# Kernel optimization log

Hardware: AMD Instinct MI355X
Metric: run time of the kernel (lower is better)

Reference implementation:

```python
import jax, jax.numpy as jnp
import numpy as np

H = 56; W = 56; WS = 7; SHIFT = 3; HEADS = 4; DIM = 128
N = WS * WS  # 49 tokens per window
EPS = 1e-5


def _rel_pos_index():
    c = np.stack(np.meshgrid(np.arange(WS), np.arange(WS), indexing='ij')).reshape(2, -1)
    r = (c[:, :, None] - c[:, None, :]).transpose(1, 2, 0)
    r[..., 0] += WS - 1
    r[..., 1] += WS - 1
    r[..., 0] *= 2 * WS - 1
    return jnp.asarray(r.sum(-1))  # [N, N] int


def _attn_mask():
    img = np.zeros((H, W))
    sl = (slice(0, -WS), slice(-WS, -SHIFT), slice(-SHIFT, None))
    cnt = 0
    for hs in sl:
        for ws_ in sl:
            img[hs, ws_] = cnt
            cnt += 1
    mw = img.reshape(H // WS, WS, W // WS, WS).transpose(0, 2, 1, 3).reshape(-1, N)
    d = mw[:, None, :] - mw[:, :, None]  # [nW, N, N]
    return jnp.asarray(np.where(d != 0, -100.0, 0.0).astype(np.float32))


def _ln(x, w, b):
    m = x.mean(-1, keepdims=True)
    v = ((x - m) ** 2).mean(-1, keepdims=True)
    return (x - m) / jnp.sqrt(v + EPS) * w + b


def setup_inputs() -> dict:
    key = jax.random.key(0)
    ks = jax.random.split(key, 8)
    B = 64
    return {
        'x': jax.random.normal(ks[0], (B, H * W, DIM), jnp.float32),
        'qkv_w': jax.random.normal(ks[1], (DIM, 3 * DIM), jnp.float32) * 0.02,
        'qkv_b': jnp.zeros((3 * DIM,), jnp.float32),
        'proj_w': jax.random.normal(ks[2], (DIM, DIM), jnp.float32) * 0.02,
        'proj_b': jnp.zeros((DIM,), jnp.float32),
        'rpb_table': jax.random.normal(ks[3], ((2 * WS - 1) ** 2, HEADS), jnp.float32) * 0.02,
        'norm1_w': jnp.ones((DIM,), jnp.float32),
        'norm1_b': jnp.zeros((DIM,), jnp.float32),
        'norm2_w': jnp.ones((DIM,), jnp.float32),
        'norm2_b': jnp.zeros((DIM,), jnp.float32),
        'mlp_w1': jax.random.normal(ks[4], (DIM, 4 * DIM), jnp.float32) * 0.02,
        'mlp_b1': jnp.zeros((4 * DIM,), jnp.float32),
        'mlp_w2': jax.random.normal(ks[5], (4 * DIM, DIM), jnp.float32) * 0.02,
        'mlp_b2': jnp.zeros((DIM,), jnp.float32),
    }


def reference(x, qkv_w, qkv_b, proj_w, proj_b, rpb_table,
              norm1_w, norm1_b, norm2_w, norm2_b,
              mlp_w1, mlp_b1, mlp_w2, mlp_b2):
    B = x.shape[0]
    C = DIM
    hd = C // HEADS
    shortcut = x
    h = _ln(x, norm1_w, norm1_b).reshape(B, H, W, C)
    # cyclic shift
    h = jnp.roll(h, (-SHIFT, -SHIFT), axis=(1, 2))
    # window partition -> [B*nW, N, C]
    xw = h.reshape(B, H // WS, WS, W // WS, WS, C).transpose(0, 1, 3, 2, 4, 5).reshape(-1, N, C)
    qkv = (xw @ qkv_w + qkv_b).reshape(-1, N, 3, HEADS, hd).transpose(2, 0, 3, 1, 4)
    q, k, v = qkv[0] * (hd ** -0.5), qkv[1], qkv[2]  # [B*nW, heads, N, hd]
    attn = jnp.einsum('whnd,whmd->whnm', q, k)
    bias = rpb_table[_rel_pos_index().reshape(-1)].reshape(N, N, HEADS).transpose(2, 0, 1)
    attn = attn + bias[None]
    mask = _attn_mask()  # [nW, N, N]
    nW = mask.shape[0]
    attn = attn.reshape(B, nW, HEADS, N, N) + mask[None, :, None]
    attn = jax.nn.softmax(attn.reshape(-1, HEADS, N, N), axis=-1)
    out = jnp.einsum('whnm,whmd->wnhd', attn, v).reshape(-1, N, C)
    out = out @ proj_w + proj_b
    # window reverse + reverse shift
    out = out.reshape(B, H // WS, W // WS, WS, WS, C).transpose(0, 1, 3, 2, 4, 5).reshape(B, H, W, C)
    out = jnp.roll(out, (SHIFT, SHIFT), axis=(1, 2)).reshape(B, H * W, C)
    x = shortcut + out
    h2 = _ln(x, norm2_w, norm2_b)
    h2 = jax.nn.gelu(h2 @ mlp_w1 + mlp_b1, approximate=False) @ mlp_w2 + mlp_b2
    return x + h2
```

## Files before the change

kernel.cpp:

```cpp
#include <hip/hip_runtime.h>

#define HH 56
#define WW2 56
#define WS 7
#define SHIFT 3
#define HEADS 4
#define DIM 128
#define NTOK 49
#define BATCH 64
#define TOKENS (BATCH*HH*WW2)
#define NWIN 64
#define WINDOWS (BATCH*NWIN)

typedef __bf16 bf16x8 __attribute__((ext_vector_type(8)));
typedef float  f32x4  __attribute__((ext_vector_type(4)));

__device__ __forceinline__ unsigned short f2bf(float f) {
  unsigned u = __float_as_uint(f);
  u += 0x7fffu + ((u >> 16) & 1u);
  return (unsigned short)(u >> 16);
}

__device__ __forceinline__ void st4(unsigned short* p, float a, float b, float c, float d) {
  ushort4 pk; pk.x = f2bf(a); pk.y = f2bf(b); pk.z = f2bf(c); pk.w = f2bf(d);
  *(ushort4*)p = pk;
}

__device__ __forceinline__ int reg3(int g) { return g >= 53 ? 2 : (g >= 49 ? 1 : 0); }

__global__ __launch_bounds__(256) void k_prep(
    const float* __restrict__ qkv_w, const float* __restrict__ proj_w,
    const float* __restrict__ w1, const float* __restrict__ w2,
    unsigned short* __restrict__ qkvwT, unsigned short* __restrict__ projwT,
    unsigned short* __restrict__ w1T, unsigned short* __restrict__ w2T)
{
  int idx = blockIdx.x * 256 + threadIdx.x;
  if (idx < 49152) {
    int n = idx >> 7, k = idx & 127;
    qkvwT[idx] = f2bf(qkv_w[k * 384 + n]);
  } else if (idx < 65536) {
    int i = idx - 49152; int n = i >> 7, k = i & 127;
    projwT[i] = f2bf(proj_w[k * 128 + n]);
  } else if (idx < 131072) {
    int i = idx - 65536; int n = i >> 7, k = i & 127;
    w1T[i] = f2bf(w1[k * 512 + n]);
  } else {
    int i = idx - 131072; int n = i >> 9, k = i & 511;
    w2T[i] = f2bf(w2[k * 128 + n]);
  }
}

__global__ __launch_bounds__(256) void k_tbl(const float* __restrict__ rpb, float* __restrict__ tbl)
{
  int idx = blockIdx.x * 256 + threadIdx.x;
  int kt = idx & 63, qt = (idx >> 6) & 63, h = (idx >> 12) & 3, cls = idx >> 14;
  float v;
  if (qt >= NTOK || kt >= NTOK) v = -3e38f;
  else {
    int qi = qt / 7, qj = qt % 7, ki = kt / 7, kj = kt % 7;
    int bi = (cls & 2) ? 49 : 0, bj = (cls & 1) ? 49 : 0;
    int rq = reg3(bi + qi) * 3 + reg3(bj + qj);
    int rk = reg3(bi + ki) * 3 + reg3(bj + kj);
    v = rpb[((qi - ki + 6) * 13 + (qj - kj + 6)) * HEADS + h] + (rq != rk ? -100.0f : 0.0f);
  }
  tbl[idx] = v;
}

__global__ __launch_bounds__(256) void k_ln1_window(
    const float* __restrict__ x, const float* __restrict__ w,
    const float* __restrict__ b, unsigned short* __restrict__ xw)
{
  int lane = threadIdx.x & 63;
  int t = blockIdx.x * 4 + (threadIdx.x >> 6);
  const float* xp = x + (size_t)t * DIM;
  float2 v = *(const float2*)(xp + lane * 2);
  float s = v.x + v.y;
  float sq = v.x * v.x + v.y * v.y;
  #pragma unroll
  for (int off = 32; off; off >>= 1) {
    s += __shfl_xor(s, off);
    sq += __shfl_xor(sq, off);
  }
  float mean = s * (1.0f / DIM);
  float var = sq * (1.0f / DIM) - mean * mean;
  float rs = rsqrtf(var + 1e-5f);
  float2 wv = *(const float2*)(w + lane * 2);
  float2 bv = *(const float2*)(b + lane * 2);
  float y0 = (v.x - mean) * rs * wv.x + bv.x;
  float y1 = (v.y - mean) * rs * wv.y + bv.y;
  int bi = t / (HH * WW2);
  int r = t % (HH * WW2);
  int i = r / WW2, j = r % WW2;
  int si = i >= SHIFT ? i - SHIFT : i + (HH - SHIFT);
  int sj = j >= SHIFT ? j - SHIFT : j + (WW2 - SHIFT);
  int win = bi * NWIN + (si / WS) * 8 + (sj / WS);
  int tok = (si % WS) * WS + (sj % WS);
  unsigned pack = ((unsigned)f2bf(y1) << 16) | (unsigned)f2bf(y0);
  *(unsigned*)(xw + ((size_t)(win * NTOK + tok)) * DIM + lane * 2) = pack;
}

__global__ __launch_bounds__(256, 2) void k_attn(
    const unsigned short* __restrict__ xw,
    const unsigned short* __restrict__ qkvwT,
    const float* __restrict__ qkv_b,
    const unsigned short* __restrict__ projwT,
    const float* __restrict__ proj_b,
    const float* __restrict__ tbl,
    unsigned short* __restrict__ attn_out)
{
  __shared__ __align__(16) unsigned short s_x[64 * 136];
  __shared__ __align__(16) unsigned short s_qk[64 * 264];
  __shared__ __align__(16) unsigned short s_vT[128 * 72];

  int tid = threadIdx.x;
  int wave = tid >> 6;
  int lane = tid & 63;
  int l = lane & 15, g = lane >> 4;
  int win = blockIdx.x;
  int wi = (win & 63) >> 3, wj = win & 7;

  const unsigned short* xwin = xw + (size_t)win * (NTOK * DIM);
  for (int idx = tid; idx < NTOK * 16; idx += 256) {
    int row = idx >> 4, seg = idx & 15;
    *(uint4*)&s_x[row * 136 + seg * 8] = *(const uint4*)(xwin + row * DIM + seg * 8);
  }
  for (int idx = tid; idx < 15 * 17; idx += 256) {
    int row = 49 + idx / 17, seg = idx % 17;
    *(uint4*)&s_x[row * 136 + seg * 8] = make_uint4(0, 0, 0, 0);
  }
  __syncthreads();

  bf16x8 xf[4][4];
  #pragma unroll
  for (int nt = 0; nt < 4; ++nt)
    #pragma unroll
    for (int kk = 0; kk < 4; ++kk)
      xf[nt][kk] = *(const bf16x8*)&s_x[(nt * 16 + l) * 136 + kk * 32 + g * 8];

  #pragma unroll
  for (int wti = 0; wti < 6; ++wti) {
    int wt = wave * 6 + wti;
    bf16x8 wf[4];
    #pragma unroll
    for (int kk = 0; kk < 4; ++kk)
      wf[kk] = *(const bf16x8*)(qkvwT + (size_t)(wt * 16 + l) * DIM + kk * 32 + g * 8);
    f32x4 acc[4];
    #pragma unroll
    for (int nt = 0; nt < 4; ++nt) acc[nt] = (f32x4){0.f, 0.f, 0.f, 0.f};
    #pragma unroll
    for (int kk = 0; kk < 4; ++kk)
      #pragma unroll
      for (int nt = 0; nt < 4; ++nt)
        acc[nt] = __builtin_amdgcn_mfma_f32_16x16x32_bf16(wf[kk], xf[nt][kk], acc[nt], 0, 0, 0);
    float4 b4 = *(const float4*)(qkv_b + wt * 16 + g * 4);
    if (wt < 16) {
      float sc = wt < 8 ? 0.17677669529663687f : 1.0f;
      #pragma unroll
      for (int nt = 0; nt < 4; ++nt)
        st4(&s_qk[(nt * 16 + l) * 264 + wt * 16 + g * 4],
            (acc[nt][0] + b4.x) * sc, (acc[nt][1] + b4.y) * sc,
            (acc[nt][2] + b4.z) * sc, (acc[nt][3] + b4.w) * sc);
    } else {
      int d0 = wt * 16 - 256 + g * 4;
      #pragma unroll
      for (int nt = 0; nt < 4; ++nt) {
        s_vT[(d0 + 0) * 72 + nt * 16 + l] = f2bf(acc[nt][0] + b4.x);
        s_vT[(d0 + 1) * 72 + nt * 16 + l] = f2bf(acc[nt][1] + b4.y);
        s_vT[(d0 + 2) * 72 + nt * 16 + l] = f2bf(acc[nt][2] + b4.z);
        s_vT[(d0 + 3) * 72 + nt * 16 + l] = f2bf(acc[nt][3] + b4.w);
      }
    }
  }
  __syncthreads();

  int h = wave;
  bf16x8 kf[4], qf[4];
  #pragma unroll
  for (int mt = 0; mt < 4; ++mt)
    kf[mt] = *(const bf16x8*)&s_qk[(mt * 16 + l) * 264 + 128 + h * 32 + g * 8];
  #pragma unroll
  for (int nt = 0; nt < 4; ++nt)
    qf[nt] = *(const bf16x8*)&s_qk[(nt * 16 + l) * 264 + h * 32 + g * 8];
  __syncthreads();

  int clsid = ((wi == 7) ? 2 : 0) | ((wj == 7) ? 1 : 0);
  const float* tb = tbl + ((clsid * 4 + h) << 12);
  f32x4 sc[4][4];
  #pragma unroll
  for (int nt = 0; nt < 4; ++nt)
    #pragma unroll
    for (int mt = 0; mt < 4; ++mt) {
      f32x4 ci = *(const f32x4*)(tb + (nt * 16 + l) * 64 + mt * 16 + g * 4);
      sc[mt][nt] = __builtin_amdgcn_mfma_f32_16x16x32_bf16(kf[mt], qf[nt], ci, 0, 0, 0);
    }

  #pragma unroll
  for (int nt = 0; nt < 4; ++nt) {
    float m = sc[0][nt][0];
    #pragma unroll
    for (int mt = 0; mt < 4; ++mt)
      #pragma unroll
      for (int rr = 0; rr < 4; ++rr) m = fmaxf(m, sc[mt][nt][rr]);
    m = fmaxf(m, __shfl_xor(m, 16));
    m = fmaxf(m, __shfl_xor(m, 32));
    float ssum = 0.f;
    #pragma unroll
    for (int mt = 0; mt < 4; ++mt)
      #pragma unroll
      for (int rr = 0; rr < 4; ++rr) {
        float e = __expf(sc[mt][nt][rr] - m);
        sc[mt][nt][rr] = e;
        ssum += e;
      }
    ssum += __shfl_xor(ssum, 16);
    ssum += __shfl_xor(ssum, 32);
    float inv = 1.0f / ssum;
    #pragma unroll
    for (int mt = 0; mt < 4; ++mt)
      st4(&s_qk[(nt * 16 + l) * 264 + h * 64 + mt * 16 + g * 4],
          sc[mt][nt][0] * inv, sc[mt][nt][1] * inv, sc[mt][nt][2] * inv, sc[mt][nt][3] * inv);
  }

  bf16x8 vf[2][2], pf[4][2];
  #pragma unroll
  for (int dt = 0; dt < 2; ++dt)
    #pragma unroll
    for (int kk = 0; kk < 2; ++kk)
      vf[dt][kk] = *(const bf16x8*)&s_vT[(h * 32 + dt * 16 + l) * 72 + kk * 32 + g * 8];
  #pragma unroll
  for (int nt = 0; nt < 4; ++nt)
    #pragma unroll
    for (int kk = 0; kk < 2; ++kk)
      pf[nt][kk] = *(const bf16x8*)&s_qk[(nt * 16 + l) * 264 + h * 64 + kk * 32 + g * 8];
  #pragma unroll
  for (int dt = 0; dt < 2; ++dt)
    #pragma unroll
    for (int nt = 0; nt < 4; ++nt) {
      f32x4 a = (f32x4){0.f, 0.f, 0.f, 0.f};
      a = __builtin_amdgcn_mfma_f32_16x16x32_bf16(vf[dt][0], pf[nt][0], a, 0, 0, 0);
      a = __builtin_amdgcn_mfma_f32_16x16x32_bf16(vf[dt][1], pf[nt][1], a, 0, 0, 0);
      st4(&s_x[(nt * 16 + l) * 136 + h * 32 + dt * 16 + g * 4], a[0], a[1], a[2], a[3]);
    }
  __syncthreads();

  unsigned short* stage = s_vT;
  bf16x8 of[4][4];
  #pragma unroll
  for (int nt = 0; nt < 4; ++nt)
    #pragma unroll
    for (int kk = 0; kk < 4; ++kk)
      of[nt][kk] = *(const bf16x8*)&s_x[(nt * 16 + l) * 136 + kk * 32 + g * 8];
  #pragma unroll
  for (int wti = 0; wti < 2; ++wti) {
    int wt = wave * 2 + wti;
    bf16x8 wf[4];
    #pragma unroll
    for (int kk = 0; kk < 4; ++kk)
      wf[kk] = *(const bf16x8*)(projwT + (size_t)(wt * 16 + l) * DIM + kk * 32 + g * 8);
    f32x4 acc[4];
    #pragma unroll
    for (int nt = 0; nt < 4; ++nt) acc[nt] = (f32x4){0.f, 0.f, 0.f, 0.f};
    #pragma unroll
    for (int kk = 0; kk < 4; ++kk)
      #pragma unroll
      for (int nt = 0; nt < 4; ++nt)
        acc[nt] = __builtin_amdgcn_mfma_f32_16x16x32_bf16(wf[kk], of[nt][kk], acc[nt], 0, 0, 0);
    float4 b4 = *(const float4*)(proj_b + wt * 16 + g * 4);
    #pragma unroll
    for (int nt = 0; nt < 4; ++nt)
      st4(&stage[(nt * 16 + l) * 136 + wt * 16 + g * 4],
          acc[nt][0] + b4.x, acc[nt][1] + b4.y, acc[nt][2] + b4.z, acc[nt][3] + b4.w);
  }
  __syncthreads();

  unsigned short* outp = attn_out + (size_t)win * (NTOK * DIM);
  for (int idx = tid; idx < NTOK * 16; idx += 256) {
    int row = idx >> 4, seg = idx & 15;
    *(uint4*)(outp + idx * 8) = *(const uint4*)&stage[row * 136 + seg * 8];
  }
}

__global__ __launch_bounds__(256) void k_resid_ln2(
    const float* __restrict__ x, const unsigned short* __restrict__ attn,
    const float* __restrict__ w, const float* __restrict__ b,
    float* __restrict__ x2, unsigned short* __restrict__ h2)
{
  int lane = threadIdx.x & 63;
  int t = blockIdx.x * 4 + (threadIdx.x >> 6);
  int bi = t / (HH * WW2);
  int r = t % (HH * WW2);
  int i = r / WW2, j = r % WW2;
  int si = i >= SHIFT ? i - SHIFT : i + (HH - SHIFT);
  int sj = j >= SHIFT ? j - SHIFT : j + (WW2 - SHIFT);
  int win = bi * NWIN + (si / WS) * 8 + (sj / WS);
  int tok = (si % WS) * WS + (sj % WS);
  float2 v = *(const float2*)(x + (size_t)t * DIM + lane * 2);
  unsigned ap = *(const unsigned*)(attn + ((size_t)(win * NTOK + tok)) * DIM + lane * 2);
  float z0 = v.x + __uint_as_float(ap << 16);
  float z1 = v.y + __uint_as_float(ap & 0xffff0000u);
  float s = z0 + z1;
  float sq = z0 * z0 + z1 * z1;
  #pragma unroll
  for (int off = 32; off; off >>= 1) {
    s += __shfl_xor(s, off);
    sq += __shfl_xor(sq, off);
  }
  float mean = s * (1.0f / DIM);
  float var = sq * (1.0f / DIM) - mean * mean;
  float rs = rsqrtf(var + 1e-5f);
  float2 wv = *(const float2*)(w + lane * 2);
  float2 bv = *(const float2*)(b + lane * 2);
  float y0 = (z0 - mean) * rs * wv.x + bv.x;
  float y1 = (z1 - mean) * rs * wv.y + bv.y;
  *(float2*)(x2 + (size_t)t * DIM + lane * 2) = make_float2(z0, z1);
  unsigned pack = ((unsigned)f2bf(y1) << 16) | (unsigned)f2bf(y0);
  *(unsigned*)(h2 + (size_t)t * DIM + lane * 2) = pack;
}

__device__ __forceinline__ float gelu_f(float x) {
  float x2 = x * x;
  float t = x * __builtin_fmaf(x2, -0.10294429f, -2.3022077f);
  float e = __builtin_amdgcn_exp2f(t);
  return x * __builtin_amdgcn_rcpf(1.0f + e);
}

__global__ __launch_bounds__(256) void k_mlp(
    const unsigned short* __restrict__ h2,
    const unsigned short* __restrict__ w1T, const float* __restrict__ b1,
    const unsigned short* __restrict__ w2T, const float* __restrict__ b2,
    float* __restrict__ io)
{
  __shared__ __align__(16) unsigned short s_t[2][64 * 136];
  int tid = threadIdx.x;
  int wave = tid >> 6;
  int lane = tid & 63;
  int l = lane & 15, g = lane >> 4;
  size_t m0 = (size_t)blockIdx.x * 64;
  const unsigned short* hp = h2 + m0 * DIM;
  for (int idx = tid; idx < 64 * 16; idx += 256) {
    int row = idx >> 4, seg = idx & 15;
    *(uint4*)&s_t[1][row * 136 + seg * 8] = *(const uint4*)(hp + row * DIM + seg * 8);
  }
  __syncthreads();

  bf16x8 hf[4][4];
  #pragma unroll
  for (int nt = 0; nt < 4; ++nt)
    #pragma unroll
    for (int kk = 0; kk < 4; ++kk)
      hf[nt][kk] = *(const bf16x8*)&s_t[1][(nt * 16 + l) * 136 + kk * 32 + g * 8];

  f32x4 o[2][4];
  #pragma unroll
  for (int wti = 0; wti < 2; ++wti)
    #pragma unroll
    for (int nt = 0; nt < 4; ++nt) o[wti][nt] = (f32x4){0.f, 0.f, 0.f, 0.f};

  for (int c = 0; c < 4; ++c) {
    unsigned short* buf = s_t[c & 1];
    #pragma unroll
    for (int wti = 0; wti < 2; ++wti) {
      int wt = wave * 2 + wti;
      int n0 = c * 128 + wt * 16;
      bf16x8 wf[4];
      #pragma unroll
      for (int kk = 0; kk < 4; ++kk)
        wf[kk] = *(const bf16x8*)(w1T + (size_t)(n0 + l) * DIM + kk * 32 + g * 8);
      f32x4 acc[4];
      #pragma unroll
      for (int nt = 0; nt < 4; ++nt) acc[nt] = (f32x4){0.f, 0.f, 0.f, 0.f};
      #pragma unroll
      for (int kk = 0; kk < 4; ++kk)
        #pragma unroll
        for (int nt = 0; nt < 4; ++nt)
          acc[nt] = __builtin_amdgcn_mfma_f32_16x16x32_bf16(wf[kk], hf[nt][kk], acc[nt], 0, 0, 0);
      float4 b4 = *(const float4*)(b1 + n0 + g * 4);
      #pragma unroll
      for (int nt = 0; nt < 4; ++nt)
        st4(&buf[(nt * 16 + l) * 136 + wt * 16 + g * 4],
            gelu_f(acc[nt][0] + b4.x), gelu_f(acc[nt][1] + b4.y),
            gelu_f(acc[nt][2] + b4.z), gelu_f(acc[nt][3] + b4.w));
    }
    __syncthreads();
    #pragma unroll
    for (int kk = 0; kk < 4; ++kk) {
      bf16x8 tf[4];
      #pragma unroll
      for (int nt = 0; nt < 4; ++nt)
        tf[nt] = *(const bf16x8*)&buf[(nt * 16 + l) * 136 + kk * 32 + g * 8];
      #pragma unroll
      for (int wti = 0; wti < 2; ++wti) {
        int wt = wave * 2 + wti;
        bf16x8 wf2 = *(const bf16x8*)(w2T + (size_t)(wt * 16 + l) * 512 + c * 128 + kk * 32 + g * 8);
        #pragma unroll
        for (int nt = 0; nt < 4; ++nt)
          o[wti][nt] = __builtin_amdgcn_mfma_f32_16x16x32_bf16(wf2, tf[nt], o[wti][nt], 0, 0, 0);
      }
    }
  }

  #pragma unroll
  for (int wti = 0; wti < 2; ++wti) {
    int wt = wave * 2 + wti;
    float4 b4 = *(const float4*)(b2 + wt * 16 + g * 4);
    #pragma unroll
    for (int nt = 0; nt < 4; ++nt) {
      float* p = io + (m0 + nt * 16 + l) * DIM + wt * 16 + g * 4;
      float4 pv = *(float4*)p;
      pv.x += o[wti][nt][0] + b4.x;
      pv.y += o[wti][nt][1] + b4.y;
      pv.z += o[wti][nt][2] + b4.z;
      pv.w += o[wti][nt][3] + b4.w;
      *(float4*)p = pv;
    }
  }
}

extern "C" void kernel_launch(void* const* d_in, const int* in_sizes, int n_in,
                              void* d_out, int out_size, void* d_ws, size_t ws_size,
                              hipStream_t stream) {
  const float* x       = (const float*)d_in[0];
  const float* qkv_w   = (const float*)d_in[1];
  const float* qkv_b   = (const float*)d_in[2];
  const float* proj_w  = (const float*)d_in[3];
  const float* proj_b  = (const float*)d_in[4];
  const float* rpb     = (const float*)d_in[5];
  const float* n1w     = (const float*)d_in[6];
  const float* n1b     = (const float*)d_in[7];
  const float* n2w     = (const float*)d_in[8];
  const float* n2b     = (const float*)d_in[9];
  const float* mlp_w1  = (const float*)d_in[10];
  const float* mlp_b1  = (const float*)d_in[11];
  const float* mlp_w2  = (const float*)d_in[12];
  const float* mlp_b2  = (const float*)d_in[13];
  float* out = (float*)d_out;

  char* ws = (char*)d_ws;
  const size_t TOKB = (size_t)TOKENS * DIM * 2;
  unsigned short* xw     = (unsigned short*)(ws);
  unsigned short* attn_o = (unsigned short*)(ws + TOKB);
  unsigned short* qkvwT  = (unsigned short*)(ws + 2 * TOKB);
  unsigned short* projwT = (unsigned short*)(ws + 2 * TOKB + 98304);
  unsigned short* w1T    = (unsigned short*)(ws + 2 * TOKB + 98304 + 32768);
  unsigned short* w2T    = (unsigned short*)(ws + 2 * TOKB + 98304 + 32768 + 131072);
  float*          tbl    = (float*)(ws + 2 * TOKB + 98304 + 32768 + 131072 + 131072);
  unsigned short* h2     = xw;

  k_prep<<<768, 256, 0, stream>>>(qkv_w, proj_w, mlp_w1, mlp_w2, qkvwT, projwT, w1T, w2T);
  k_tbl<<<256, 256, 0, stream>>>(rpb, tbl);
  k_ln1_window<<<TOKENS / 4, 256, 0, stream>>>(x, n1w, n1b, xw);
  k_attn<<<WINDOWS, 256, 0, stream>>>(xw, qkvwT, qkv_b, projwT, proj_b, tbl, attn_o);
  k_resid_ln2<<<TOKENS / 4, 256, 0, stream>>>(x, attn_o, n2w, n2b, out, h2);
  k_mlp<<<TOKENS / 64, 256, 0, stream>>>(h2, w1T, mlp_b1, w2T, mlp_b2, out);
}
```

Measured before the change: 527.7 us.

## Fuse residual add and LayerNorm2 into the MLP kernel prologue

Removes the separate residual+LN2 kernel. The MLP kernel now gathers the attention output through the reverse window/shift mapping, adds the shortcut, writes x2 to the output buffer, and computes the LayerNorm statistics with a cross-wave reduction in shared memory before writing the bf16 normalized tile into LDS. This drops one kernel launch and the global write and re-read of the bf16 h2 tensor. In exchange the MLP kernel gains a more complex prologue with an extra barrier and more registers held per thread.

```diff
diff --git a/kernel.cpp b/kernel.cpp
--- a/kernel.cpp
+++ b/kernel.cpp
@@ -280,43 +280,6 @@
   }
 }
 
-__global__ __launch_bounds__(256) void k_resid_ln2(
-    const float* __restrict__ x, const unsigned short* __restrict__ attn,
-    const float* __restrict__ w, const float* __restrict__ b,
-    float* __restrict__ x2, unsigned short* __restrict__ h2)
-{
-  int lane = threadIdx.x & 63;
-  int t = blockIdx.x * 4 + (threadIdx.x >> 6);
-  int bi = t / (HH * WW2);
-  int r = t % (HH * WW2);
-  int i = r / WW2, j = r % WW2;
-  int si = i >= SHIFT ? i - SHIFT : i + (HH - SHIFT);
-  int sj = j >= SHIFT ? j - SHIFT : j + (WW2 - SHIFT);
-  int win = bi * NWIN + (si / WS) * 8 + (sj / WS);
-  int tok = (si % WS) * WS + (sj % WS);
-  float2 v = *(const float2*)(x + (size_t)t * DIM + lane * 2);
-  unsigned ap = *(const unsigned*)(attn + ((size_t)(win * NTOK + tok)) * DIM + lane * 2);
-  float z0 = v.x + __uint_as_float(ap << 16);
-  float z1 = v.y + __uint_as_float(ap & 0xffff0000u);
-  float s = z0 + z1;
-  float sq = z0 * z0 + z1 * z1;
-  #pragma unroll
-  for (int off = 32; off; off >>= 1) {
-    s += __shfl_xor(s, off);
-    sq += __shfl_xor(sq, off);
-  }
-  float mean = s * (1.0f / DIM);
-  float var = sq * (1.0f / DIM) - mean * mean;
-  float rs = rsqrtf(var + 1e-5f);
-  float2 wv = *(const float2*)(w + lane * 2);
-  float2 bv = *(const float2*)(b + lane * 2);
-  float y0 = (z0 - mean) * rs * wv.x + bv.x;
-  float y1 = (z1 - mean) * rs * wv.y + bv.y;
-  *(float2*)(x2 + (size_t)t * DIM + lane * 2) = make_float2(z0, z1);
-  unsigned pack = ((unsigned)f2bf(y1) << 16) | (unsigned)f2bf(y0);
-  *(unsigned*)(h2 + (size_t)t * DIM + lane * 2) = pack;
-}
-
 __device__ __forceinline__ float gelu_f(float x) {
   float x2 = x * x;
   float t = x * __builtin_fmaf(x2, -0.10294429f, -2.3022077f);
@@ -325,21 +288,84 @@
 }
 
 __global__ __launch_bounds__(256) void k_mlp(
-    const unsigned short* __restrict__ h2,
+    const float* __restrict__ x, const unsigned short* __restrict__ attn,
+    const float* __restrict__ n2w, const float* __restrict__ n2b,
     const unsigned short* __restrict__ w1T, const float* __restrict__ b1,
     const unsigned short* __restrict__ w2T, const float* __restrict__ b2,
     float* __restrict__ io)
 {
   __shared__ __align__(16) unsigned short s_t[2][64 * 136];
+  __shared__ float s_part[64][4][2];
   int tid = threadIdx.x;
   int wave = tid >> 6;
   int lane = tid & 63;
   int l = lane & 15, g = lane >> 4;
   size_t m0 = (size_t)blockIdx.x * 64;
-  const unsigned short* hp = h2 + m0 * DIM;
-  for (int idx = tid; idx < 64 * 16; idx += 256) {
-    int row = idx >> 4, seg = idx & 15;
-    *(uint4*)&s_t[1][row * 136 + seg * 8] = *(const uint4*)(hp + row * DIM + seg * 8);
+  int col0 = wave * 32 + g * 4;
+
+  float4 xz[4][2];
+  float sA[4], sQ[4];
+  #pragma unroll
+  for (int nt = 0; nt < 4; ++nt) {
+    int row = nt * 16 + l;
+    int t = (int)m0 + row;
+    int bi = t / (HH * WW2);
+    int r = t % (HH * WW2);
+    int i = r / WW2, j = r % WW2;
+    int si = i >= SHIFT ? i - SHIFT : i + (HH - SHIFT);
+    int sj = j >= SHIFT ? j - SHIFT : j + (WW2 - SHIFT);
+    int win = bi * NWIN + (si / WS) * 8 + (sj / WS);
+    int tok = (si % WS) * WS + (sj % WS);
+    const float* xp = x + (size_t)t * DIM;
+    const unsigned short* ap = attn + ((size_t)(win * NTOK + tok)) * DIM;
+    float s = 0.f, sq = 0.f;
+    #pragma unroll
+    for (int wti = 0; wti < 2; ++wti) {
+      int col = col0 + wti * 16;
+      float4 xv = *(const float4*)(xp + col);
+      ushort4 av = *(const ushort4*)(ap + col);
+      float4 z;
+      z.x = xv.x + __uint_as_float((unsigned)av.x << 16);
+      z.y = xv.y + __uint_as_float((unsigned)av.y << 16);
+      z.z = xv.z + __uint_as_float((unsigned)av.z << 16);
+      z.w = xv.w + __uint_as_float((unsigned)av.w << 16);
+      xz[nt][wti] = z;
+      s += z.x + z.y + z.z + z.w;
+      sq += z.x * z.x + z.y * z.y + z.z * z.z + z.w * z.w;
+      *(float4*)(io + (size_t)t * DIM + col) = z;
+    }
+    s += __shfl_xor(s, 16); s += __shfl_xor(s, 32);
+    sq += __shfl_xor(sq, 16); sq += __shfl_xor(sq, 32);
+    sA[nt] = s; sQ[nt] = sq;
+  }
+  if (g == 0) {
+    #pragma unroll
+    for (int nt = 0; nt < 4; ++nt) {
+      s_part[nt * 16 + l][wave][0] = sA[nt];
+      s_part[nt * 16 + l][wave][1] = sQ[nt];
+    }
+  }
+  __syncthreads();
+  float4 wv0 = *(const float4*)(n2w + col0);
+  float4 wv1 = *(const float4*)(n2w + col0 + 16);
+  float4 bv0 = *(const float4*)(n2b + col0);
+  float4 bv1 = *(const float4*)(n2b + col0 + 16);
+  #pragma unroll
+  for (int nt = 0; nt < 4; ++nt) {
+    int row = nt * 16 + l;
+    float s = 0.f, sq = 0.f;
+    #pragma unroll
+    for (int wv = 0; wv < 4; ++wv) { s += s_part[row][wv][0]; sq += s_part[row][wv][1]; }
+    float mean = s * (1.0f / DIM);
+    float var = sq * (1.0f / DIM) - mean * mean;
+    float rs = rsqrtf(var + 1e-5f);
+    float4 z0 = xz[nt][0], z1 = xz[nt][1];
+    st4(&s_t[1][row * 136 + col0],
+        (z0.x - mean) * rs * wv0.x + bv0.x, (z0.y - mean) * rs * wv0.y + bv0.y,
+        (z0.z - mean) * rs * wv0.z + bv0.z, (z0.w - mean) * rs * wv0.w + bv0.w);
+    st4(&s_t[1][row * 136 + col0 + 16],
+        (z1.x - mean) * rs * wv1.x + bv1.x, (z1.y - mean) * rs * wv1.y + bv1.y,
+        (z1.z - mean) * rs * wv1.z + bv1.z, (z1.w - mean) * rs * wv1.w + bv1.w);
   }
   __syncthreads();
 
@@ -444,12 +470,10 @@
   unsigned short* w1T    = (unsigned short*)(ws + 2 * TOKB + 98304 + 32768);
   unsigned short* w2T    = (unsigned short*)(ws + 2 * TOKB + 98304 + 32768 + 131072);
   float*          tbl    = (float*)(ws + 2 * TOKB + 98304 + 32768 + 131072 + 131072);
-  unsigned short* h2     = xw;
 
   k_prep<<<768, 256, 0, stream>>>(qkv_w, proj_w, mlp_w1, mlp_w2, qkvwT, projwT, w1T, w2T);
   k_tbl<<<256, 256, 0, stream>>>(rpb, tbl);
   k_ln1_window<<<TOKENS / 4, 256, 0, stream>>>(x, n1w, n1b, xw);
   k_attn<<<WINDOWS, 256, 0, stream>>>(xw, qkvwT, qkv_b, projwT, proj_b, tbl, attn_o);
-  k_resid_ln2<<<TOKENS / 4, 256, 0, stream>>>(x, attn_o, n2w, n2b, out, h2);
-  k_mlp<<<TOKENS / 64, 256, 0, stream>>>(h2, w1T, mlp_b1, w2T, mlp_b2, out);
-}
+  k_mlp<<<TOKENS / 64, 256, 0, stream>>>(x, attn_o, n2w, n2b, w1T, mlp_b1, w2T, mlp_b2, out);
+}
```

After: 500.2 us. 5.2% less time.
